# Optimization experiments

Hardware: AMD Instinct MI355X
Metric: run time of the kernel (lower is better)

Reference implementation:

```python
import jax, jax.numpy as jnp
import numpy as np

RES = 16; NC = 256; NCP = 1024; KNN = 32; SIGMA = 0.1
DM = 256; NH = 8; FF = 1024; NLAYERS = 2
E = NC * 8 * (RES // 8) ** 2
EH = 8
B = 4; N = 65536


def setup_inputs() -> dict:
    key = jax.random.key(0)
    ks = jax.random.split(key, 16)
    s = 0.02
    def w(k, shape):
        return jax.random.normal(k, shape, jnp.float32) * s
    inp = {}
    inp['pc'] = jax.random.normal(ks[0], (B, N, 3), jnp.float32)
    inp['pe_w1'] = w(ks[1], (3, 128)); inp['pe_b1'] = jnp.zeros((128,), jnp.float32)
    inp['pe_w2'] = w(ks[2], (128, 128)); inp['pe_b2'] = jnp.zeros((128,), jnp.float32)
    inp['t_qkv_w'] = w(ks[3], (NLAYERS, DM, 3 * DM)); inp['t_qkv_b'] = jnp.zeros((NLAYERS, 3 * DM), jnp.float32)
    inp['t_out_w'] = w(ks[4], (NLAYERS, DM, DM)); inp['t_out_b'] = jnp.zeros((NLAYERS, DM), jnp.float32)
    inp['t_ln1_s'] = jnp.ones((NLAYERS, DM), jnp.float32); inp['t_ln1_b'] = jnp.zeros((NLAYERS, DM), jnp.float32)
    inp['t_ff1_w'] = w(ks[5], (NLAYERS, DM, FF)); inp['t_ff1_b'] = jnp.zeros((NLAYERS, FF), jnp.float32)
    inp['t_ff2_w'] = w(ks[6], (NLAYERS, FF, DM)); inp['t_ff2_b'] = jnp.zeros((NLAYERS, DM), jnp.float32)
    inp['t_ln2_s'] = jnp.ones((NLAYERS, DM), jnp.float32); inp['t_ln2_b'] = jnp.zeros((NLAYERS, DM), jnp.float32)
    inp['c1_w'] = w(ks[7], (2 * NC, NC, 3, 3)); inp['c1_b'] = jnp.zeros((2 * NC,), jnp.float32)
    inp['c2_w'] = w(ks[8], (4 * NC, 2 * NC, 3, 3)); inp['c2_b'] = jnp.zeros((4 * NC,), jnp.float32)
    inp['c3_w'] = w(ks[9], (8 * NC, 4 * NC, 3, 3)); inp['c3_b'] = jnp.zeros((8 * NC,), jnp.float32)
    inp['x_qkv_w'] = w(ks[10], (E, 3 * E)); inp['x_qkv_b'] = jnp.zeros((3 * E,), jnp.float32)
    inp['x_out_w'] = w(ks[11], (E, E)); inp['x_out_b'] = jnp.zeros((E,), jnp.float32)
    return inp


def _layernorm(x, s, b):
    m = x.mean(-1, keepdims=True)
    v = ((x - m) ** 2).mean(-1, keepdims=True)
    return (x - m) / jnp.sqrt(v + 1e-5) * s + b


def _mha(x, qkv_w, qkv_b, out_w, out_b, nh):
    Bq, S, D = x.shape
    dh = D // nh
    qkv = x @ qkv_w + qkv_b
    q, k, v = jnp.split(qkv, 3, axis=-1)
    def sp(t):
        return t.reshape(Bq, S, nh, dh).transpose(0, 2, 1, 3)
    q, k, v = sp(q), sp(k), sp(v)
    a = jax.nn.softmax(jnp.einsum('bhqd,bhkd->bhqk', q, k) / jnp.sqrt(jnp.float32(dh)), axis=-1)
    o = jnp.einsum('bhqk,bhkd->bhqd', a, v).transpose(0, 2, 1, 3).reshape(Bq, S, D)
    return o @ out_w + out_b


def _density(pc):
    # faithful to source: distance to the FIRST k points (unsorted), not kNN
    d = jnp.linalg.norm(pc[:, :, None, :] - pc[:, None, :KNN, :], axis=-1)  # (B,N,k)
    return jnp.exp(-2.0 * SIGMA ** 2 / (d * d + 1e-6)).mean(axis=-1)


def _fps_indices(pc, density):
    # incremental min-dist FPS: selects identical points to the original O(N*K^2) loop
    def one(pc_b, dens_b):
        first = jnp.argmax(dens_b)
        mind = jnp.linalg.norm(pc_b - pc_b[first], axis=-1)
        def step(mind, _):
            idx = jnp.argmax(mind)
            d = jnp.linalg.norm(pc_b - pc_b[idx], axis=-1)
            return jnp.minimum(mind, d), idx
        _, rest = jax.lax.scan(step, mind, None, length=NCP - 1)
        return jnp.concatenate([first[None], rest])
    return jax.vmap(one)(pc, density)


def _forward(pc, idx, pe_w1, pe_b1, pe_w2, pe_b2, t_qkv_w, t_qkv_b, t_out_w, t_out_b,
             t_ln1_s, t_ln1_b, t_ff1_w, t_ff1_b, t_ff2_w, t_ff2_b, t_ln2_s, t_ln2_b,
             c1_w, c1_b, c2_w, c2_b, c3_w, c3_b, x_qkv_w, x_qkv_b, x_out_w, x_out_b):
    Bq = pc.shape[0]
    centers = jnp.take_along_axis(pc, idx[:, :, None], axis=1)  # (B,K,3)
    # point encoder MLP -> (B,K,128)
    f = jax.nn.relu(centers @ pe_w1 + pe_b1) @ pe_w2 + pe_b2
    # sinusoidal pos-emb per axis, mean over xyz -> (B,K,128)
    half = 64
    freqs = jnp.exp(jnp.arange(half, dtype=jnp.float32) * (-np.log(10000.0) / (half - 1)))
    e = centers[..., None] * freqs  # (B,K,3,64)
    pos = jnp.concatenate([jnp.sin(e), jnp.cos(e)], axis=-1).mean(axis=2)
    x = jnp.concatenate([f, pos], axis=-1)  # (B,K,256)
    # 2-layer post-LN transformer encoder
    for l in range(NLAYERS):
        h = _mha(x, t_qkv_w[l], t_qkv_b[l], t_out_w[l], t_out_b[l], NH)
        x = _layernorm(x + h, t_ln1_s[l], t_ln1_b[l])
        h = jax.nn.relu(x @ t_ff1_w[l] + t_ff1_b[l]) @ t_ff2_w[l] + t_ff2_b[l]
        x = _layernorm(x + h, t_ln2_s[l], t_ln2_b[l])
    # scatter-add features onto three planes
    L = pc.max() - pc.min()
    def grid(c):
        return jnp.clip(((c + L / 2) / L * RES).astype(jnp.int32), 0, RES - 1)
    gx = grid(centers[..., 0]); gy = grid(centers[..., 1]); gz = grid(centers[..., 2])
    tri = jnp.zeros((Bq, 3, RES, RES, DM), jnp.float32)  # channels last for scatter
    bi = jnp.arange(Bq)[:, None]
    tri = tri.at[bi, 0, gy, gx].add(x)
    tri = tri.at[bi, 1, gz, gy].add(x)
    tri = tri.at[bi, 2, gz, gx].add(x)
    tri = tri.transpose(0, 1, 4, 2, 3)  # (B,3,C,R,R)
    z = tri.reshape(Bq * 3, DM, RES, RES)
    def conv(xx, w, b):
        y = jax.lax.conv_general_dilated(xx, w, (2, 2), ((1, 1), (1, 1)),
                                         dimension_numbers=('NCHW', 'OIHW', 'NCHW'))
        return y + b[None, :, None, None]
    z = jax.nn.relu(conv(z, c1_w, c1_b))
    z = jax.nn.relu(conv(z, c2_w, c2_b))
    z = jax.nn.relu(conv(z, c3_w, c3_b))  # (B*3, 8C, R/8, R/8)
    flat = z.reshape(Bq, 3, E)
    attn = _mha(flat, x_qkv_w, x_qkv_b, x_out_w, x_out_b, EH)
    return attn.reshape(Bq, 3, 8 * NC, RES // 8, RES // 8)


def reference(pc, pe_w1, pe_b1, pe_w2, pe_b2, t_qkv_w, t_qkv_b, t_out_w, t_out_b,
              t_ln1_s, t_ln1_b, t_ff1_w, t_ff1_b, t_ff2_w, t_ff2_b, t_ln2_s, t_ln2_b,
              c1_w, c1_b, c2_w, c2_b, c3_w, c3_b, x_qkv_w, x_qkv_b, x_out_w, x_out_b):
    idx = _fps_indices(pc, _density(pc))
    return _forward(pc, idx, pe_w1, pe_b1, pe_w2, pe_b2, t_qkv_w, t_qkv_b, t_out_w, t_out_b,
                    t_ln1_s, t_ln1_b, t_ff1_w, t_ff1_b, t_ff2_w, t_ff2_b, t_ln2_s, t_ln2_b,
                    c1_w, c1_b, c2_w, c2_b, c3_w, c3_b, x_qkv_w, x_qkv_b, x_out_w, x_out_b)
```

## Files before the change

### kernel.cpp

```cpp
#include <hip/hip_runtime.h>
#include <math.h>

#define NPTS   65536
#define NBATCH 4
#define KCP    1024
#define DM     256
#define FFD    1024
#define EDIM   8192
#define N3E    24576

#define FPS_NBLK 16
#define FPS_THR  256
#define FPS_PPT  16
#define GPUB     8
#define HARV_MAX 16
#define RING     16

typedef __attribute__((ext_vector_type(8))) short short8v;
typedef __attribute__((ext_vector_type(4))) short short4v;
typedef __attribute__((ext_vector_type(4))) float float4v;

__device__ __forceinline__ unsigned long long umaxll(unsigned long long a, unsigned long long b) {
  return a > b ? a : b;
}

__device__ __forceinline__ short bf16rn(float f) {
  unsigned u = __float_as_uint(f);
  return (short)((u + 0x7FFFu + ((u >> 16) & 1u)) >> 16);
}

__global__ __launch_bounds__(256) void redmm_kernel(const float* __restrict__ v, int n,
                                                    float* __restrict__ pmax, float* __restrict__ pmin) {
  float mx = -INFINITY, mn = INFINITY;
  for (int i = blockIdx.x * 256 + threadIdx.x; i < n; i += gridDim.x * 256) {
    float x = v[i]; mx = fmaxf(mx, x); mn = fminf(mn, x);
  }
#pragma unroll
  for (int off = 32; off >= 1; off >>= 1) {
    mx = fmaxf(mx, __shfl_xor(mx, off, 64));
    mn = fminf(mn, __shfl_xor(mn, off, 64));
  }
  __shared__ float smx[4], smn[4];
  int lane = threadIdx.x & 63, w = threadIdx.x >> 6;
  if (lane == 0) { smx[w] = mx; smn[w] = mn; }
  __syncthreads();
  if (threadIdx.x == 0) {
    pmax[blockIdx.x] = fmaxf(fmaxf(smx[0], smx[1]), fmaxf(smx[2], smx[3]));
    pmin[blockIdx.x] = fminf(fminf(smn[0], smn[1]), fminf(smn[2], smn[3]));
  }
}

__global__ __launch_bounds__(256) void redfin_kernel(const float* __restrict__ pmax,
                                                     const float* __restrict__ pmin, int nb,
                                                     float* __restrict__ Lv) {
  float mx = -INFINITY, mn = INFINITY;
  for (int i = threadIdx.x; i < nb; i += 256) { mx = fmaxf(mx, pmax[i]); mn = fminf(mn, pmin[i]); }
#pragma unroll
  for (int off = 32; off >= 1; off >>= 1) {
    mx = fmaxf(mx, __shfl_xor(mx, off, 64));
    mn = fminf(mn, __shfl_xor(mn, off, 64));
  }
  __shared__ float smx[4], smn[4];
  int lane = threadIdx.x & 63, w = threadIdx.x >> 6;
  if (lane == 0) { smx[w] = mx; smn[w] = mn; }
  __syncthreads();
  if (threadIdx.x == 0) {
    mx = fmaxf(fmaxf(smx[0], smx[1]), fmaxf(smx[2], smx[3]));
    mn = fminf(fminf(smn[0], smn[1]), fminf(smn[2], smn[3]));
    Lv[0] = __fsub_rn(mx, mn);
  }
}

__global__ __launch_bounds__(FPS_THR, 1) void fps_kernel(const float* __restrict__ pc,
                                                         float* __restrict__ centers,
                                                         unsigned* __restrict__ tags,
                                                         unsigned long long* __restrict__ keys) {
  const int blk = blockIdx.x;
  const int b = blk / FPS_NBLK, bb = blk % FPS_NBLK;
  const int tid = threadIdx.x;
  const int lane = tid & 63, wv = tid >> 6;
  const int wvg = bb * 4 + wv;
  const float* pcb = pc + (size_t)b * NPTS * 3;

  __shared__ float kpts[96];

  float px[FPS_PPT], py[FPS_PPT], pz[FPS_PPT], mind[FPS_PPT];
  const int gbase = wvg * 1024;
#pragma unroll
  for (int i = 0; i < FPS_PPT; ++i) {
    int g = gbase + i * 64 + lane;
    px[i] = pcb[3 * g]; py[i] = pcb[3 * g + 1]; pz[i] = pcb[3 * g + 2];
  }
  for (int i = tid; i < 96; i += FPS_THR) kpts[i] = pcb[i];
  __syncthreads();

  unsigned* const tagb = tags + (size_t)b * RING * 64;
  unsigned long long* const keyb = keys + (size_t)b * RING * 64 * GPUB;

  auto exchange = [&](const unsigned long long* ek, int nk, int r,
                      unsigned long long* ck) {
    const int ri = r & (RING - 1);
    if (lane == 0) {
      unsigned long long* sp = keyb + ((size_t)ri * 64 + wvg) * GPUB;
      for (int g = 0; g < nk; ++g)
        __hip_atomic_store(&sp[g], ek[g], __ATOMIC_RELAXED, __HIP_MEMORY_SCOPE_AGENT);
      __hip_atomic_store(&tagb[ri * 64 + wvg], (unsigned)r, __ATOMIC_RELEASE, __HIP_MEMORY_SCOPE_AGENT);
    }
    unsigned tag;
    do {
      tag = __hip_atomic_load(&tagb[ri * 64 + lane], __ATOMIC_ACQUIRE, __HIP_MEMORY_SCOPE_AGENT);
    } while (__any(tag != (unsigned)r));
    const unsigned long long* pl = keyb + ((size_t)ri * 64 + lane) * GPUB;
    for (int e = 0; e < nk; ++e)
      ck[e] = __hip_atomic_load(&pl[e], __ATOMIC_RELAXED, __HIP_MEMORY_SCOPE_AGENT);
  };

  {
    unsigned long long bk = 0ull;
#pragma unroll
    for (int i = 0; i < FPS_PPT; ++i) {
      float acc = 0.f;
      for (int j = 0; j < 32; ++j) {
        float dx = __fsub_rn(px[i], kpts[3 * j]);
        float dy = __fsub_rn(py[i], kpts[3 * j + 1]);
        float dz = __fsub_rn(pz[i], kpts[3 * j + 2]);
        float ss = __fadd_rn(__fadd_rn(__fmul_rn(dx, dx), __fmul_rn(dy, dy)), __fmul_rn(dz, dz));
        float d = __fsqrt_rn(ss);
        float dd = __fadd_rn(__fmul_rn(d, d), 1e-6f);
        acc = __fadd_rn(acc, expf(__fdiv_rn(-0.02f, dd)));
      }
      float dens = __fdiv_rn(acc, 32.f);
      int g = gbase + i * 64 + lane;
      bk = umaxll(bk, ((unsigned long long)__float_as_uint(dens) << 32) | (unsigned int)(~g));
    }
#pragma unroll
    for (int off = 1; off < 64; off <<= 1) bk = umaxll(bk, __shfl_xor(bk, off, 64));
    unsigned long long ek[1] = { bk }, ck[1];
    exchange(ek, 1, 1, ck);
    unsigned long long k2 = ck[0];
#pragma unroll
    for (int off = 1; off < 64; off <<= 1) k2 = umaxll(k2, __shfl_xor(k2, off, 64));
    int widx = (int)(~(unsigned)(k2 & 0xFFFFFFFFull));
    float wx = pcb[3 * widx], wy = pcb[3 * widx + 1], wz = pcb[3 * widx + 2];
    if (wvg == 0 && lane == 0) {
      centers[(size_t)b * KCP * 3 + 0] = wx;
      centers[(size_t)b * KCP * 3 + 1] = wy;
      centers[(size_t)b * KCP * 3 + 2] = wz;
    }
#pragma unroll
    for (int i = 0; i < FPS_PPT; ++i) {
      float dx = __fsub_rn(px[i], wx), dy = __fsub_rn(py[i], wy), dz = __fsub_rn(pz[i], wz);
      mind[i] = __fsqrt_rn(__fadd_rn(__fadd_rn(__fmul_rn(dx, dx), __fmul_rn(dy, dy)), __fmul_rn(dz, dz)));
    }
  }

  int t = 1;
  for (int r = 2; t < KCP; ++r) {
    unsigned long long tk[FPS_PPT];
#pragma unroll
    for (int i = 0; i < FPS_PPT; ++i) {
      int g = gbase + i * 64 + lane;
      tk[i] = ((unsigned long long)__float_as_uint(mind[i]) << 32) | (unsigned int)(~g);
    }
    unsigned long long ek[GPUB];
#pragma unroll
    for (int g = 0; g < GPUB; ++g) {
      unsigned long long lbk = 0ull;
#pragma unroll
      for (int i = 0; i < FPS_PPT; ++i) lbk = umaxll(lbk, tk[i]);
      unsigned long long wk = lbk;
#pragma unroll
      for (int off = 1; off < 64; off <<= 1) wk = umaxll(wk, __shfl_xor(wk, off, 64));
      ek[g] = wk;
#pragma unroll
      for (int i = 0; i < FPS_PPT; ++i)
        if (tk[i] == wk) tk[i] = 0ull;
    }
    unsigned long long ck[GPUB];
    exchange(ek, GPUB, r, ck);
    float cx[GPUB], cy[GPUB], cz[GPUB];
#pragma unroll
    for (int e = 0; e < GPUB; ++e) {
      int gi = (int)(~(unsigned)(ck[e] & 0xFFFFFFFFull));
      cx[e] = pcb[3 * gi]; cy[e] = pcb[3 * gi + 1]; cz[e] = pcb[3 * gi + 2];
    }
    unsigned long long u = ck[GPUB - 1];
#pragma unroll
    for (int off = 1; off < 64; off <<= 1) u = umaxll(u, __shfl_xor(u, off, 64));
    int h = 0;
    while (true) {
      unsigned long long lb = 0ull; float lx = 0.f, ly = 0.f, lz = 0.f;
#pragma unroll
      for (int e = 0; e < GPUB; ++e)
        if (ck[e] > lb) { lb = ck[e]; lx = cx[e]; ly = cy[e]; lz = cz[e]; }
      unsigned long long wk = lb;
#pragma unroll
      for (int off = 1; off < 64; off <<= 1) wk = umaxll(wk, __shfl_xor(wk, off, 64));
      if (h > 0 && wk < u) break;
      int owner = __ffsll(__ballot(lb == wk)) - 1;
      float wx = __shfl(lx, owner, 64), wy = __shfl(ly, owner, 64), wz = __shfl(lz, owner, 64);
      if (wvg == 0 && lane == 0) {
        centers[((size_t)b * KCP + t) * 3 + 0] = wx;
        centers[((size_t)b * KCP + t) * 3 + 1] = wy;
        centers[((size_t)b * KCP + t) * 3 + 2] = wz;
      }
#pragma unroll
      for (int e = 0; e < GPUB; ++e) {
        float dx = __fsub_rn(cx[e], wx), dy = __fsub_rn(cy[e], wy), dz = __fsub_rn(cz[e], wz);
        float d = __fsqrt_rn(__fadd_rn(__fadd_rn(__fmul_rn(dx, dx), __fmul_rn(dy, dy)), __fmul_rn(dz, dz)));
        float ov = __uint_as_float((unsigned)(ck[e] >> 32));
        float nv = fminf(ov, d);
        ck[e] = ((unsigned long long)__float_as_uint(nv) << 32) | (ck[e] & 0xFFFFFFFFull);
      }
#pragma unroll
      for (int i = 0; i < FPS_PPT; ++i) {
        float dx = __fsub_rn(px[i], wx), dy = __fsub_rn(py[i], wy), dz = __fsub_rn(pz[i], wz);
        float d = __fsqrt_rn(__fadd_rn(__fadd_rn(__fmul_rn(dx, dx), __fmul_rn(dy, dy)), __fmul_rn(dz, dz)));
        mind[i] = fminf(mind[i], d);
      }
      ++h; ++t;
      if (h == HARV_MAX || t == KCP) break;
    }
  }
}

__global__ __launch_bounds__(128) void pe_kernel(const float* __restrict__ centers,
                                                 const float* __restrict__ w1, const float* __restrict__ b1,
                                                 const float* __restrict__ w2, const float* __restrict__ b2,
                                                 float* __restrict__ x) {
  const int p = blockIdx.x;
  const int d = threadIdx.x;
  __shared__ float h[128];
  __shared__ float c[3];
  if (d < 3) c[d] = centers[(size_t)p * 3 + d];
  __syncthreads();
  float hv = b1[d];
#pragma unroll
  for (int j = 0; j < 3; ++j) hv += c[j] * w1[j * 128 + d];
  hv = fmaxf(hv, 0.f);
  h[d] = hv;
  __syncthreads();
  float f = b2[d];
  for (int j = 0; j < 128; ++j) f += h[j] * w2[j * 128 + d];
  x[(size_t)p * 256 + d] = f;
  if (d < 64) {
    float fr = expf(__fmul_rn((float)d, -0.14619587892025696f));
    float ssum = 0.f, csum = 0.f;
#pragma unroll
    for (int a = 0; a < 3; ++a) {
      float e = __fmul_rn(c[a], fr);
      ssum += sinf(e); csum += cosf(e);
    }
    x[(size_t)p * 256 + 128 + d] = __fdiv_rn(ssum, 3.f);
    x[(size_t)p * 256 + 192 + d] = __fdiv_rn(csum, 3.f);
  }
}

__global__ __launch_bounds__(256) void gemm_mfma_kernel(const float* __restrict__ A,
                                                        const float* __restrict__ W,
                                                        const float* __restrict__ bias,
                                                        float* __restrict__ C,
                                                        int M, int Kd, int Nd, int relu) {
  __shared__ __align__(16) short Al[128][40];
  __shared__ __align__(16) short Wl[128][40];
  const int bm = blockIdx.y * 128, bn = blockIdx.x * 128;
  const int tid = threadIdx.x;
  const int lane = tid & 63, wv = tid >> 6;
  const int wr = wv >> 1, wc = wv & 1;
  const int l15 = lane & 15, lk = lane >> 4;

  float4v acc[4][4];
#pragma unroll
  for (int i = 0; i < 4; ++i)
#pragma unroll
    for (int j = 0; j < 4; ++j) acc[i][j] = (float4v){0.f, 0.f, 0.f, 0.f};

  for (int k0 = 0; k0 < Kd; k0 += 32) {
    __syncthreads();
#pragma unroll
    for (int i = 0; i < 4; ++i) {
      int idx = (i * 256 + tid) * 4;
      int m = idx >> 5, k = idx & 31;
      float4 v = *(const float4*)&A[(size_t)(bm + m) * Kd + k0 + k];
      short4v s = { bf16rn(v.x), bf16rn(v.y), bf16rn(v.z), bf16rn(v.w) };
      *(short4v*)&Al[m][k] = s;
    }
#pragma unroll
    for (int i = 0; i < 4; ++i) {
      int task = i * 256 + tid;
      int n = task & 127, c = task >> 7;
      short4v s;
#pragma unroll
      for (int j = 0; j < 4; ++j)
        s[j] = bf16rn(W[(size_t)(k0 + c * 4 + j) * Nd + bn + n]);
      *(short4v*)&Wl[n][c * 4] = s;
    }
    __syncthreads();
    short8v af[4], bf[4];
#pragma unroll
    for (int mf = 0; mf < 4; ++mf)
      af[mf] = *(const short8v*)&Al[wr * 64 + mf * 16 + l15][lk * 8];
#pragma unroll
    for (int nf = 0; nf < 4; ++nf)
      bf[nf] = *(const short8v*)&Wl[wc * 64 + nf * 16 + l15][lk * 8];
#pragma unroll
    for (int mf = 0; mf < 4; ++mf)
#pragma unroll
      for (int nf = 0; nf < 4; ++nf)
        acc[mf][nf] = __builtin_amdgcn_mfma_f32_16x16x32_bf16(af[mf], bf[nf], acc[mf][nf], 0, 0, 0);
  }

#pragma unroll
  for (int mf = 0; mf < 4; ++mf) {
    int row = bm + wr * 64 + mf * 16 + lk * 4;
#pragma unroll
    for (int nf = 0; nf < 4; ++nf) {
      int col = bn + wc * 64 + nf * 16 + l15;
      float bv = bias[col];
#pragma unroll
      for (int j = 0; j < 4; ++j) {
        float v = acc[mf][nf][j] + bv;
        if (relu) v = fmaxf(v, 0.f);
        C[(size_t)(row + j) * Nd + col] = v;
      }
    }
  }
}

__global__ __launch_bounds__(256, 1) void flash_mfma_kernel(const float* __restrict__ qkv,
                                                            float* __restrict__ ao) {
  const int qt = blockIdx.x, h = blockIdx.y, b = blockIdx.z;
  const int tid = threadIdx.x;
  const int lane = tid & 63, w = tid >> 6;
  const int l15 = lane & 15, lk = lane >> 4;
  const int q0 = qt * 64;

  __shared__ __align__(16) short Kc[64][40];
  __shared__ __align__(16) short Vt[32][72];
  __shared__ __align__(16) short Plds[4][16][72];

  short8v qa;
  {
    const float* qr = qkv + (size_t)(b * 1024 + q0 + w * 16 + l15) * 768 + h * 32 + lk * 8;
    float4 a = *(const float4*)qr;
    float4 c = *(const float4*)(qr + 4);
    qa = (short8v){ bf16rn(a.x), bf16rn(a.y), bf16rn(a.z), bf16rn(a.w),
                    bf16rn(c.x), bf16rn(c.y), bf16rn(c.z), bf16rn(c.w) };
  }

  float4v o0 = (float4v){0.f, 0.f, 0.f, 0.f};
  float4v o1 = (float4v){0.f, 0.f, 0.f, 0.f};
  float m_cur[4] = { -INFINITY, -INFINITY, -INFINITY, -INFINITY };
  float l_part[4] = { 0.f, 0.f, 0.f, 0.f };
  const float scale = 0.17677669529663687f;

  for (int c0 = 0; c0 < 1024; c0 += 64) {
    __syncthreads();
    {
      int key = tid >> 2, dblk = (tid & 3) * 8;
      size_t row = (size_t)(b * 1024 + c0 + key) * 768 + h * 32 + dblk;
      float4 k1 = *(const float4*)&qkv[row + 256];
      float4 k2 = *(const float4*)&qkv[row + 260];
      short8v ks = (short8v){ bf16rn(k1.x), bf16rn(k1.y), bf16rn(k1.z), bf16rn(k1.w),
                              bf16rn(k2.x), bf16rn(k2.y), bf16rn(k2.z), bf16rn(k2.w) };
      *(short8v*)&Kc[key][dblk] = ks;
      float4 v1 = *(const float4*)&qkv[row + 512];
      float4 v2 = *(const float4*)&qkv[row + 516];
      Vt[dblk + 0][key] = bf16rn(v1.x); Vt[dblk + 1][key] = bf16rn(v1.y);
      Vt[dblk + 2][key] = bf16rn(v1.z); Vt[dblk + 3][key] = bf16rn(v1.w);
      Vt[dblk + 4][key] = bf16rn(v2.x); Vt[dblk + 5][key] = bf16rn(v2.y);
      Vt[dblk + 6][key] = bf16rn(v2.z); Vt[dblk + 7][key] = bf16rn(v2.w);
    }
    __syncthreads();

    float4v s[4];
#pragma unroll
    for (int f = 0; f < 4; ++f) {
      short8v kb = *(const short8v*)&Kc[f * 16 + l15][lk * 8];
      float4v z = (float4v){0.f, 0.f, 0.f, 0.f};
      s[f] = __builtin_amdgcn_mfma_f32_16x16x32_bf16(qa, kb, z, 0, 0, 0);
    }
#pragma unroll
    for (int f = 0; f < 4; ++f)
#pragma unroll
      for (int j = 0; j < 4; ++j) s[f][j] *= scale;

    float corr[4];
#pragma unroll
    for (int j = 0; j < 4; ++j) {
      float v = fmaxf(fmaxf(s[0][j], s[1][j]), fmaxf(s[2][j], s[3][j]));
#pragma unroll
      for (int off = 1; off < 16; off <<= 1) v = fmaxf(v, __shfl_xor(v, off, 64));
      float m_new = fmaxf(m_cur[j], v);
      corr[j] = expf(m_cur[j] - m_new);
      m_cur[j] = m_new;
    }
#pragma unroll
    for (int f = 0; f < 4; ++f)
#pragma unroll
      for (int j = 0; j < 4; ++j) {
        float p = expf(s[f][j] - m_cur[j]);
        s[f][j] = p;
        Plds[w][lk * 4 + j][f * 16 + l15] = bf16rn(p);
      }
#pragma unroll
    for (int j = 0; j < 4; ++j) {
      float tsum = s[0][j] + s[1][j] + s[2][j] + s[3][j];
#pragma unroll
      for (int off = 1; off < 16; off <<= 1) tsum += __shfl_xor(tsum, off, 64);
      l_part[j] = l_part[j] * corr[j] + tsum;
      o0[j] *= corr[j];
      o1[j] *= corr[j];
    }
    asm volatile("s_waitcnt lgkmcnt(0)" ::: "memory");
    __builtin_amdgcn_sched_barrier(0);

#pragma unroll
    for (int kb = 0; kb < 2; ++kb) {
      short8v pa = *(const short8v*)&Plds[w][l15][kb * 32 + lk * 8];
      short8v vb0 = *(const short8v*)&Vt[l15][kb * 32 + lk * 8];
      short8v vb1 = *(const short8v*)&Vt[16 + l15][kb * 32 + lk * 8];
      o0 = __builtin_amdgcn_mfma_f32_16x16x32_bf16(pa, vb0, o0, 0, 0, 0);
      o1 = __builtin_amdgcn_mfma_f32_16x16x32_bf16(pa, vb1, o1, 0, 0, 0);
    }
  }

#pragma unroll
  for (int j = 0; j < 4; ++j) {
    float inv = 1.f / l_part[j];
    int q = q0 + w * 16 + lk * 4 + j;
    float* orow = ao + (size_t)(b * 1024 + q) * 256 + h * 32;
    orow[l15] = o0[j] * inv;
    orow[16 + l15] = o1[j] * inv;
  }
}

__global__ __launch_bounds__(256) void ln_kernel(const float* __restrict__ a, const float* __restrict__ r,
                                                 const float* __restrict__ sc, const float* __restrict__ bi,
                                                 float* __restrict__ out) {
  const int row = blockIdx.x * 4 + (threadIdx.x >> 6);
  const int lane = threadIdx.x & 63;
  const float* ar = a + (size_t)row * 256;
  const float* rr = r + (size_t)row * 256;
  float v[4];
#pragma unroll
  for (int i = 0; i < 4; ++i) v[i] = ar[lane + 64 * i] + rr[lane + 64 * i];
  float s = v[0] + v[1] + v[2] + v[3];
#pragma unroll
  for (int off = 32; off >= 1; off >>= 1) s += __shfl_xor(s, off, 64);
  float mean = s * (1.f / 256.f);
  float vs = 0.f;
#pragma unroll
  for (int i = 0; i < 4; ++i) { float d = v[i] - mean; vs += d * d; }
#pragma unroll
  for (int off = 32; off >= 1; off >>= 1) vs += __shfl_xor(vs, off, 64);
  float var = vs * (1.f / 256.f);
  float rstd = 1.f / sqrtf(var + 1e-5f);
  float* orow = out + (size_t)row * 256;
#pragma unroll
  for (int i = 0; i < 4; ++i) {
    int d = lane + 64 * i;
    orow[d] = (v[i] - mean) * rstd * sc[d] + bi[d];
  }
}

__global__ __launch_bounds__(256) void scatter_kernel(const float* __restrict__ x,
                                                      const float* __restrict__ centers,
                                                      const float* __restrict__ Lv,
                                                      float* __restrict__ tri) {
  const int pnt = blockIdx.x;
  const int b = pnt >> 10;
  const int tid = threadIdx.x;
  __shared__ int g[3];
  if (tid == 0) {
    float L = Lv[0];
    float half = __fmul_rn(L, 0.5f);
#pragma unroll
    for (int a = 0; a < 3; ++a) {
      float c = centers[(size_t)pnt * 3 + a];
      float t = __fmul_rn(__fdiv_rn(__fadd_rn(c, half), L), 16.f);
      int gi = (int)t;
      g[a] = min(15, max(0, gi));
    }
  }
  __syncthreads();
  const int gx = g[0], gy = g[1], gz = g[2];
  float v = x[(size_t)pnt * 256 + tid];
  float* trib = tri + (size_t)b * 3 * 256 * 256;
  atomicAdd(&trib[(0 * 256 + tid) * 256 + gy * 16 + gx], v);
  atomicAdd(&trib[(1 * 256 + tid) * 256 + gz * 16 + gy], v);
  atomicAdd(&trib[(2 * 256 + tid) * 256 + gz * 16 + gx], v);
}

template <int IC, int OC, int IH, int IW, int OH, int OW, int OCT, int ICC>
__global__ __launch_bounds__(256, 1) void conv_kernel(const float* __restrict__ in, const float* __restrict__ w,
                                                      const float* __restrict__ bias, float* __restrict__ out) {
  __shared__ float lin[ICC * IH * IW];
  const int n = blockIdx.x;
  const int oc = blockIdx.y * OCT + threadIdx.x / (OH * OW);
  const int sp = threadIdx.x % (OH * OW);
  const int oy = sp / OW, ox = sp % OW;
  const int iy0 = oy * 2 - 1, ix0 = ox * 2 - 1;
  float acc = 0.f;
  for (int c0 = 0; c0 < IC; c0 += ICC) {
    __syncthreads();
    for (int i = threadIdx.x; i < ICC * IH * IW; i += 256)
      lin[i] = in[((size_t)n * IC + c0) * (IH * IW) + i];
    __syncthreads();
    const float* wp = w + ((size_t)oc * IC + c0) * 9;
    for (int ic = 0; ic < ICC; ++ic) {
      const float* wr = wp + (size_t)ic * 9;
      const float* lr = lin + ic * IH * IW;
#pragma unroll
      for (int ky = 0; ky < 3; ++ky) {
        int iy = iy0 + ky;
        if (iy >= 0 && iy < IH) {
#pragma unroll
          for (int kx = 0; kx < 3; ++kx) {
            int ix = ix0 + kx;
            if (ix >= 0 && ix < IW) acc += lr[iy * IW + ix] * wr[ky * 3 + kx];
          }
        }
      }
    }
  }
  out[((size_t)n * OC + oc) * (OH * OW) + sp] = fmaxf(acc + bias[oc], 0.f);
}

__global__ void biasinit_kernel(float* __restrict__ out, const float* __restrict__ bias, int M, int N) {
  int i = blockIdx.x * 256 + threadIdx.x;
  if (i < M * N) out[i] = bias[i % N];
}

template <int M, int KC>
__global__ __launch_bounds__(256, 1) void matvec_kernel(const float* __restrict__ A, const float* __restrict__ W,
                                                        float* __restrict__ out, int Kd, int Nd) {
  __shared__ float Al[KC * M];
  const int tid = threadIdx.x;
  const int n = blockIdx.x * 256 + tid;
  const int k0 = blockIdx.y * KC;
  for (int i = tid; i < KC * M; i += 256) {
    int k = i / M, m = i - k * M;
    Al[i] = A[(size_t)m * Kd + k0 + k];
  }
  __syncthreads();
  float acc[M] = {};
  for (int k = 0; k < KC; ++k) {
    float wv = W[(size_t)(k0 + k) * Nd + n];
#pragma unroll
    for (int m = 0; m < M; ++m) acc[m] += Al[k * M + m] * wv;
  }
#pragma unroll
  for (int m = 0; m < M; ++m) atomicAdd(&out[(size_t)m * Nd + n], acc[m]);
}

__global__ __launch_bounds__(256) void attn3_kernel(const float* __restrict__ qkv, float* __restrict__ o) {
  const int b = blockIdx.x >> 3, h = blockIdx.x & 7;
  const float* base = qkv + (size_t)b * 3 * N3E;
  const int qo = h * 1024, ko = EDIM + h * 1024, vo = 2 * EDIM + h * 1024;
  float p[9] = {};
  for (int d = threadIdx.x; d < 1024; d += 256) {
    float q0 = base[qo + d], q1 = base[N3E + qo + d], q2 = base[2 * N3E + qo + d];
    float k0 = base[ko + d], k1 = base[N3E + ko + d], k2 = base[2 * N3E + ko + d];
    p[0] += q0 * k0; p[1] += q0 * k1; p[2] += q0 * k2;
    p[3] += q1 * k0; p[4] += q1 * k1; p[5] += q1 * k2;
    p[6] += q2 * k0; p[7] += q2 * k1; p[8] += q2 * k2;
  }
  __shared__ float red[4][9];
  __shared__ float aw[9];
  const int lane = threadIdx.x & 63, w = threadIdx.x >> 6;
#pragma unroll
  for (int e = 0; e < 9; ++e)
#pragma unroll
    for (int off = 32; off >= 1; off >>= 1) p[e] += __shfl_xor(p[e], off, 64);
  if (lane == 0)
#pragma unroll
    for (int e = 0; e < 9; ++e) red[w][e] = p[e];
  __syncthreads();
  if (threadIdx.x == 0) {
    float s[9];
#pragma unroll
    for (int e = 0; e < 9; ++e) s[e] = (red[0][e] + red[1][e] + red[2][e] + red[3][e]) / 32.f;
#pragma unroll
    for (int i = 0; i < 3; ++i) {
      float m = fmaxf(fmaxf(s[i * 3], s[i * 3 + 1]), s[i * 3 + 2]);
      float e0 = expf(s[i * 3] - m), e1 = expf(s[i * 3 + 1] - m), e2 = expf(s[i * 3 + 2] - m);
      float sm = e0 + e1 + e2;
      aw[i * 3] = e0 / sm; aw[i * 3 + 1] = e1 / sm; aw[i * 3 + 2] = e2 / sm;
    }
  }
  __syncthreads();
  for (int d = threadIdx.x; d < 1024; d += 256) {
    float v0 = base[vo + d], v1 = base[N3E + vo + d], v2 = base[2 * N3E + vo + d];
#pragma unroll
    for (int i = 0; i < 3; ++i)
      o[(size_t)(b * 3 + i) * EDIM + h * 1024 + d] = aw[i * 3] * v0 + aw[i * 3 + 1] * v1 + aw[i * 3 + 2] * v2;
  }
}

extern "C" void kernel_launch(void* const* d_in, const int* in_sizes, int n_in,
                              void* d_out, int out_size, void* d_ws, size_t ws_size,
                              hipStream_t stream) {
  const float* pc      = (const float*)d_in[0];
  const float* pe_w1   = (const float*)d_in[1];
  const float* pe_b1   = (const float*)d_in[2];
  const float* pe_w2   = (const float*)d_in[3];
  const float* pe_b2   = (const float*)d_in[4];
  const float* t_qkv_w = (const float*)d_in[5];
  const float* t_qkv_b = (const float*)d_in[6];
  const float* t_out_w = (const float*)d_in[7];
  const float* t_out_b = (const float*)d_in[8];
  const float* t_ln1_s = (const float*)d_in[9];
  const float* t_ln1_b = (const float*)d_in[10];
  const float* t_ff1_w = (const float*)d_in[11];
  const float* t_ff1_b = (const float*)d_in[12];
  const float* t_ff2_w = (const float*)d_in[13];
  const float* t_ff2_b = (const float*)d_in[14];
  const float* t_ln2_s = (const float*)d_in[15];
  const float* t_ln2_b = (const float*)d_in[16];
  const float* c1_w    = (const float*)d_in[17];
  const float* c1_b    = (const float*)d_in[18];
  const float* c2_w    = (const float*)d_in[19];
  const float* c2_b    = (const float*)d_in[20];
  const float* c3_w    = (const float*)d_in[21];
  const float* c3_b    = (const float*)d_in[22];
  const float* x_qkv_w = (const float*)d_in[23];
  const float* x_qkv_b = (const float*)d_in[24];
  const float* x_out_w = (const float*)d_in[25];
  const float* x_out_b = (const float*)d_in[26];
  float* outp = (float*)d_out;

  char* wsp = (char*)d_ws;
  auto alloc = [&](size_t bytes) { char* q = wsp; wsp += (bytes + 255) & ~(size_t)255; return q; };
  float* centers = (float*)alloc((size_t)NBATCH * KCP * 3 * 4);
  float* pmax    = (float*)alloc(512 * 4);
  float* pmin    = (float*)alloc(512 * 4);
  float* Lv      = (float*)alloc(256);
  unsigned* tags = (unsigned*)alloc((size_t)NBATCH * RING * 64 * 4);
  unsigned long long* keyss = (unsigned long long*)alloc((size_t)NBATCH * RING * 64 * GPUB * 8);
  float* x  = (float*)alloc((size_t)4096 * 256 * 4);
  float* xb = (float*)alloc((size_t)4096 * 256 * 4);
  float* arena = (float*)wsp;
  float* qkvb = arena;
  float* ao   = qkvb + (size_t)4096 * 768;
  float* po   = ao + (size_t)4096 * 256;
  float* ffh  = po + (size_t)4096 * 256;
  float* ffo  = ffh + (size_t)4096 * 1024;
  float* tri  = arena;
  float* z1   = tri + (size_t)NBATCH * 3 * 256 * 256;
  float* z2   = z1 + (size_t)12 * 512 * 64;
  float* z3   = z2 + (size_t)12 * 1024 * 16;
  float* qkv2 = z3 + (size_t)12 * 8192;
  float* at2  = qkv2 + (size_t)12 * N3E;
  (void)in_sizes; (void)n_in; (void)out_size; (void)ws_size; (void)ffo;

  hipMemsetAsync(tags, 0, (size_t)NBATCH * RING * 64 * 4, stream);
  hipMemsetAsync(keyss, 0, (size_t)NBATCH * RING * 64 * GPUB * 8, stream);

  redmm_kernel<<<512, 256, 0, stream>>>(pc, NBATCH * NPTS * 3, pmax, pmin);
  redfin_kernel<<<1, 256, 0, stream>>>(pmax, pmin, 512, Lv);

  fps_kernel<<<NBATCH * FPS_NBLK, FPS_THR, 0, stream>>>(pc, centers, tags, keyss);

  pe_kernel<<<NBATCH * KCP, 128, 0, stream>>>(centers, pe_w1, pe_b1, pe_w2, pe_b2, x);

  for (int l = 0; l < 2; ++l) {
    gemm_mfma_kernel<<<dim3(6, 32), 256, 0, stream>>>(x, t_qkv_w + (size_t)l * 256 * 768,
                                                      t_qkv_b + (size_t)l * 768, qkvb, 4096, 256, 768, 0);
    flash_mfma_kernel<<<dim3(16, 8, 4), 256, 0, stream>>>(qkvb, ao);
    gemm_mfma_kernel<<<dim3(2, 32), 256, 0, stream>>>(ao, t_out_w + (size_t)l * 256 * 256,
                                                      t_out_b + (size_t)l * 256, po, 4096, 256, 256, 0);
    ln_kernel<<<1024, 256, 0, stream>>>(x, po, t_ln1_s + (size_t)l * 256, t_ln1_b + (size_t)l * 256, xb);
    gemm_mfma_kernel<<<dim3(8, 32), 256, 0, stream>>>(xb, t_ff1_w + (size_t)l * 256 * 1024,
                                                      t_ff1_b + (size_t)l * 1024, ffh, 4096, 256, 1024, 1);
    gemm_mfma_kernel<<<dim3(2, 32), 256, 0, stream>>>(ffh, t_ff2_w + (size_t)l * 1024 * 256,
                                                      t_ff2_b + (size_t)l * 256, ffo, 4096, 1024, 256, 0);
    ln_kernel<<<1024, 256, 0, stream>>>(xb, ffo, t_ln2_s + (size_t)l * 256, t_ln2_b + (size_t)l * 256, x);
  }

  hipMemsetAsync(tri, 0, (size_t)NBATCH * 3 * 256 * 256 * 4, stream);
  scatter_kernel<<<NBATCH * KCP, 256, 0, stream>>>(x, centers, Lv, tri);

  conv_kernel<256, 512, 16, 16, 8, 8, 4, 32><<<dim3(12, 128), 256, 0, stream>>>(tri, c1_w, c1_b, z1);
  conv_kernel<512, 1024, 8, 8, 4, 4, 16, 128><<<dim3(12, 64), 256, 0, stream>>>(z1, c2_w, c2_b, z2);
  conv_kernel<1024, 2048, 4, 4, 2, 2, 64, 256><<<dim3(12, 32), 256, 0, stream>>>(z2, c3_w, c3_b, z3);

  biasinit_kernel<<<(12 * N3E + 255) / 256, 256, 0, stream>>>(qkv2, x_qkv_b, 12, N3E);
  matvec_kernel<12, 512><<<dim3(N3E / 256, 16), 256, 0, stream>>>(z3, x_qkv_w, qkv2, EDIM, N3E);

  attn3_kernel<<<32, 256, 0, stream>>>(qkv2, at2);

  biasinit_kernel<<<(12 * EDIM + 255) / 256, 256, 0, stream>>>(outp, x_out_b, 12, EDIM);
  matvec_kernel<12, 512><<<dim3(EDIM / 256, 16), 256, 0, stream>>>(at2, x_out_w, outp, EDIM, EDIM);
}
```

Measured before the change: 4.824 ms.

## Poll FPS exchange from one wave per block and split FPS into two launches

Only wave 0 of each block now spins on the inter-block tag ring and performs the greedy harvest of candidate centers. The winners are shared with the other waves through shared memory after a block barrier. This removes redundant polling and duplicate harvest work across the four waves. FPS is also split into two launches at a midpoint, persisting per-point min distances and round/count state in a workspace buffer. This adds a launch, a save/restore of state and a per-round __syncthreads.

```diff
diff --git a/kernel.cpp b/kernel.cpp
--- a/kernel.cpp
+++ b/kernel.cpp
@@ -15,6 +15,7 @@
 #define GPUB     8
 #define HARV_MAX 16
 #define RING     16
+#define TSPLIT   512
 
 typedef __attribute__((ext_vector_type(8))) short short8v;
 typedef __attribute__((ext_vector_type(4))) short short4v;
@@ -74,7 +75,10 @@
 __global__ __launch_bounds__(FPS_THR, 1) void fps_kernel(const float* __restrict__ pc,
                                                          float* __restrict__ centers,
                                                          unsigned* __restrict__ tags,
-                                                         unsigned long long* __restrict__ keys) {
+                                                         unsigned long long* __restrict__ keys,
+                                                         float* __restrict__ mindbuf,
+                                                         int* __restrict__ state,
+                                                         int phase) {
   const int blk = blockIdx.x;
   const int b = blk / FPS_NBLK, bb = blk % FPS_NBLK;
   const int tid = threadIdx.x;
@@ -83,6 +87,8 @@
   const float* pcb = pc + (size_t)b * NPTS * 3;
 
   __shared__ float kpts[96];
+  __shared__ float wlds[2][HARV_MAX][3];
+  __shared__ int hcnt[2];
 
   float px[FPS_PPT], py[FPS_PPT], pz[FPS_PPT], mind[FPS_PPT];
   const int gbase = wvg * 1024;
@@ -91,31 +97,15 @@
     int g = gbase + i * 64 + lane;
     px[i] = pcb[3 * g]; py[i] = pcb[3 * g + 1]; pz[i] = pcb[3 * g + 2];
   }
-  for (int i = tid; i < 96; i += FPS_THR) kpts[i] = pcb[i];
-  __syncthreads();
 
   unsigned* const tagb = tags + (size_t)b * RING * 64;
   unsigned long long* const keyb = keys + (size_t)b * RING * 64 * GPUB;
-
-  auto exchange = [&](const unsigned long long* ek, int nk, int r,
-                      unsigned long long* ck) {
-    const int ri = r & (RING - 1);
-    if (lane == 0) {
-      unsigned long long* sp = keyb + ((size_t)ri * 64 + wvg) * GPUB;
-      for (int g = 0; g < nk; ++g)
-        __hip_atomic_store(&sp[g], ek[g], __ATOMIC_RELAXED, __HIP_MEMORY_SCOPE_AGENT);
-      __hip_atomic_store(&tagb[ri * 64 + wvg], (unsigned)r, __ATOMIC_RELEASE, __HIP_MEMORY_SCOPE_AGENT);
-    }
-    unsigned tag;
-    do {
-      tag = __hip_atomic_load(&tagb[ri * 64 + lane], __ATOMIC_ACQUIRE, __HIP_MEMORY_SCOPE_AGENT);
-    } while (__any(tag != (unsigned)r));
-    const unsigned long long* pl = keyb + ((size_t)ri * 64 + lane) * GPUB;
-    for (int e = 0; e < nk; ++e)
-      ck[e] = __hip_atomic_load(&pl[e], __ATOMIC_RELAXED, __HIP_MEMORY_SCOPE_AGENT);
-  };
-
-  {
+  float* const mb = mindbuf + ((size_t)b * 64 + wvg) * FPS_PPT * 64;
+
+  int t, r;
+  if (phase == 0) {
+    for (int i = tid; i < 96; i += FPS_THR) kpts[i] = pcb[i];
+    __syncthreads();
     unsigned long long bk = 0ull;
 #pragma unroll
     for (int i = 0; i < FPS_PPT; ++i) {
@@ -135,9 +125,16 @@
     }
 #pragma unroll
     for (int off = 1; off < 64; off <<= 1) bk = umaxll(bk, __shfl_xor(bk, off, 64));
-    unsigned long long ek[1] = { bk }, ck[1];
-    exchange(ek, 1, 1, ck);
-    unsigned long long k2 = ck[0];
+    if (lane == 0) {
+      keyb[(size_t)(1 & (RING - 1)) * 64 * GPUB + wvg * GPUB] = bk;
+      __hip_atomic_store(&tagb[(1 & (RING - 1)) * 64 + wvg], 1u, __ATOMIC_RELEASE, __HIP_MEMORY_SCOPE_AGENT);
+    }
+    unsigned tag;
+    do {
+      tag = __hip_atomic_load(&tagb[(1 & (RING - 1)) * 64 + lane], __ATOMIC_ACQUIRE, __HIP_MEMORY_SCOPE_AGENT);
+    } while (__any(tag != 1u));
+    unsigned long long k2 = __hip_atomic_load(&keyb[(size_t)(1 & (RING - 1)) * 64 * GPUB + lane * GPUB],
+                                              __ATOMIC_RELAXED, __HIP_MEMORY_SCOPE_AGENT);
 #pragma unroll
     for (int off = 1; off < 64; off <<= 1) k2 = umaxll(k2, __shfl_xor(k2, off, 64));
     int widx = (int)(~(unsigned)(k2 & 0xFFFFFFFFull));
@@ -152,10 +149,15 @@
       float dx = __fsub_rn(px[i], wx), dy = __fsub_rn(py[i], wy), dz = __fsub_rn(pz[i], wz);
       mind[i] = __fsqrt_rn(__fadd_rn(__fadd_rn(__fmul_rn(dx, dx), __fmul_rn(dy, dy)), __fmul_rn(dz, dz)));
     }
-  }
-
-  int t = 1;
-  for (int r = 2; t < KCP; ++r) {
+    t = 1; r = 2;
+  } else {
+    r = state[b * 2]; t = state[b * 2 + 1];
+#pragma unroll
+    for (int i = 0; i < FPS_PPT; ++i) mind[i] = mb[i * 64 + lane];
+  }
+
+  const int tend = phase ? KCP : TSPLIT;
+  while (t < tend) {
     unsigned long long tk[FPS_PPT];
 #pragma unroll
     for (int i = 0; i < FPS_PPT; ++i) {
@@ -176,51 +178,85 @@
       for (int i = 0; i < FPS_PPT; ++i)
         if (tk[i] == wk) tk[i] = 0ull;
     }
-    unsigned long long ck[GPUB];
-    exchange(ek, GPUB, r, ck);
-    float cx[GPUB], cy[GPUB], cz[GPUB];
-#pragma unroll
-    for (int e = 0; e < GPUB; ++e) {
-      int gi = (int)(~(unsigned)(ck[e] & 0xFFFFFFFFull));
-      cx[e] = pcb[3 * gi]; cy[e] = pcb[3 * gi + 1]; cz[e] = pcb[3 * gi + 2];
-    }
-    unsigned long long u = ck[GPUB - 1];
-#pragma unroll
-    for (int off = 1; off < 64; off <<= 1) u = umaxll(u, __shfl_xor(u, off, 64));
-    int h = 0;
-    while (true) {
-      unsigned long long lb = 0ull; float lx = 0.f, ly = 0.f, lz = 0.f;
+    const int ri = r & (RING - 1);
+    if (lane == 0) {
+      unsigned long long* sp = keyb + ((size_t)ri * 64 + wvg) * GPUB;
+#pragma unroll
+      for (int g = 0; g < GPUB; ++g)
+        __hip_atomic_store(&sp[g], ek[g], __ATOMIC_RELAXED, __HIP_MEMORY_SCOPE_AGENT);
+      __hip_atomic_store(&tagb[ri * 64 + wvg], (unsigned)r, __ATOMIC_RELEASE, __HIP_MEMORY_SCOPE_AGENT);
+    }
+
+    if (wv == 0) {
+      unsigned tag;
+      do {
+        tag = __hip_atomic_load(&tagb[ri * 64 + lane], __ATOMIC_ACQUIRE, __HIP_MEMORY_SCOPE_AGENT);
+      } while (__any(tag != (unsigned)r));
+      const unsigned long long* pl = keyb + ((size_t)ri * 64 + lane) * GPUB;
+      unsigned long long ck[GPUB];
 #pragma unroll
       for (int e = 0; e < GPUB; ++e)
-        if (ck[e] > lb) { lb = ck[e]; lx = cx[e]; ly = cy[e]; lz = cz[e]; }
-      unsigned long long wk = lb;
-#pragma unroll
-      for (int off = 1; off < 64; off <<= 1) wk = umaxll(wk, __shfl_xor(wk, off, 64));
-      if (h > 0 && wk < u) break;
-      int owner = __ffsll(__ballot(lb == wk)) - 1;
-      float wx = __shfl(lx, owner, 64), wy = __shfl(ly, owner, 64), wz = __shfl(lz, owner, 64);
-      if (wvg == 0 && lane == 0) {
-        centers[((size_t)b * KCP + t) * 3 + 0] = wx;
-        centers[((size_t)b * KCP + t) * 3 + 1] = wy;
-        centers[((size_t)b * KCP + t) * 3 + 2] = wz;
+        ck[e] = __hip_atomic_load(&pl[e], __ATOMIC_RELAXED, __HIP_MEMORY_SCOPE_AGENT);
+      float cx[GPUB], cy[GPUB], cz[GPUB];
+#pragma unroll
+      for (int e = 0; e < GPUB; ++e) {
+        int gi = (int)(~(unsigned)(ck[e] & 0xFFFFFFFFull));
+        cx[e] = pcb[3 * gi]; cy[e] = pcb[3 * gi + 1]; cz[e] = pcb[3 * gi + 2];
       }
-#pragma unroll
-      for (int e = 0; e < GPUB; ++e) {
-        float dx = __fsub_rn(cx[e], wx), dy = __fsub_rn(cy[e], wy), dz = __fsub_rn(cz[e], wz);
-        float d = __fsqrt_rn(__fadd_rn(__fadd_rn(__fmul_rn(dx, dx), __fmul_rn(dy, dy)), __fmul_rn(dz, dz)));
-        float ov = __uint_as_float((unsigned)(ck[e] >> 32));
-        float nv = fminf(ov, d);
-        ck[e] = ((unsigned long long)__float_as_uint(nv) << 32) | (ck[e] & 0xFFFFFFFFull);
+      unsigned long long u = ck[GPUB - 1];
+#pragma unroll
+      for (int off = 1; off < 64; off <<= 1) u = umaxll(u, __shfl_xor(u, off, 64));
+      int h = 0, tl = t;
+      while (true) {
+        unsigned long long lb = 0ull; float lx = 0.f, ly = 0.f, lz = 0.f;
+#pragma unroll
+        for (int e = 0; e < GPUB; ++e)
+          if (ck[e] > lb) { lb = ck[e]; lx = cx[e]; ly = cy[e]; lz = cz[e]; }
+        unsigned long long wk = lb;
+#pragma unroll
+        for (int off = 1; off < 64; off <<= 1) wk = umaxll(wk, __shfl_xor(wk, off, 64));
+        if (h > 0 && wk < u) break;
+        int owner = __ffsll(__ballot(lb == wk)) - 1;
+        float wx = __shfl(lx, owner, 64), wy = __shfl(ly, owner, 64), wz = __shfl(lz, owner, 64);
+        if (lane == 0) {
+          wlds[r & 1][h][0] = wx; wlds[r & 1][h][1] = wy; wlds[r & 1][h][2] = wz;
+          if (bb == 0) {
+            centers[((size_t)b * KCP + tl) * 3 + 0] = wx;
+            centers[((size_t)b * KCP + tl) * 3 + 1] = wy;
+            centers[((size_t)b * KCP + tl) * 3 + 2] = wz;
+          }
+        }
+#pragma unroll
+        for (int e = 0; e < GPUB; ++e) {
+          float dx = __fsub_rn(cx[e], wx), dy = __fsub_rn(cy[e], wy), dz = __fsub_rn(cz[e], wz);
+          float d = __fsqrt_rn(__fadd_rn(__fadd_rn(__fmul_rn(dx, dx), __fmul_rn(dy, dy)), __fmul_rn(dz, dz)));
+          float ov = __uint_as_float((unsigned)(ck[e] >> 32));
+          float nv = fminf(ov, d);
+          ck[e] = ((unsigned long long)__float_as_uint(nv) << 32) | (ck[e] & 0xFFFFFFFFull);
+        }
+        ++h; ++tl;
+        if (h == HARV_MAX || tl == KCP) break;
       }
+      if (lane == 0) hcnt[r & 1] = h;
+    }
+    __syncthreads();
+    const int h = hcnt[r & 1];
+    for (int j = 0; j < h; ++j) {
+      float wx = wlds[r & 1][j][0], wy = wlds[r & 1][j][1], wz = wlds[r & 1][j][2];
 #pragma unroll
       for (int i = 0; i < FPS_PPT; ++i) {
         float dx = __fsub_rn(px[i], wx), dy = __fsub_rn(py[i], wy), dz = __fsub_rn(pz[i], wz);
         float d = __fsqrt_rn(__fadd_rn(__fadd_rn(__fmul_rn(dx, dx), __fmul_rn(dy, dy)), __fmul_rn(dz, dz)));
         mind[i] = fminf(mind[i], d);
       }
-      ++h; ++t;
-      if (h == HARV_MAX || t == KCP) break;
-    }
+    }
+    t += h; ++r;
+  }
+
+  if (phase == 0) {
+#pragma unroll
+    for (int i = 0; i < FPS_PPT; ++i) mb[i * 64 + lane] = mind[i];
+    if (bb == 0 && wv == 0 && lane == 0) { state[b * 2] = r; state[b * 2 + 1] = t; }
   }
 }
 
@@ -638,6 +674,8 @@
   float* Lv      = (float*)alloc(256);
   unsigned* tags = (unsigned*)alloc((size_t)NBATCH * RING * 64 * 4);
   unsigned long long* keyss = (unsigned long long*)alloc((size_t)NBATCH * RING * 64 * GPUB * 8);
+  float* mindbuf = (float*)alloc((size_t)NBATCH * NPTS * 4);
+  int* fstate    = (int*)alloc(256);
   float* x  = (float*)alloc((size_t)4096 * 256 * 4);
   float* xb = (float*)alloc((size_t)4096 * 256 * 4);
   float* arena = (float*)wsp;
@@ -660,7 +698,8 @@
   redmm_kernel<<<512, 256, 0, stream>>>(pc, NBATCH * NPTS * 3, pmax, pmin);
   redfin_kernel<<<1, 256, 0, stream>>>(pmax, pmin, 512, Lv);
 
-  fps_kernel<<<NBATCH * FPS_NBLK, FPS_THR, 0, stream>>>(pc, centers, tags, keyss);
+  fps_kernel<<<NBATCH * FPS_NBLK, FPS_THR, 0, stream>>>(pc, centers, tags, keyss, mindbuf, fstate, 0);
+  fps_kernel<<<NBATCH * FPS_NBLK, FPS_THR, 0, stream>>>(pc, centers, tags, keyss, mindbuf, fstate, 1);
 
   pe_kernel<<<NBATCH * KCP, 128, 0, stream>>>(centers, pe_w1, pe_b1, pe_w2, pe_b2, x);
 
```

Result: faster. 4.511 ms (-6.5%).
